# Optimization experiments

Hardware: AMD Instinct MI355X
Metric: run time of the kernel (lower is better)

The kernel has to match this reference:

```python
import jax, jax.numpy as jnp
import numpy as np

# MoE combine: for each sorted row r, output[token_indices[r]] += sorted_gates[r] * expert_outputs[r]
# The EP all_reduce is a sum over the expert-parallel mesh; on a single device it is the identity.

def setup_inputs() -> dict:
    key = jax.random.key(0)
    k1, k2, k3 = jax.random.split(key, 3)
    NUM_TOKENS = 16384   # batch 4 * seq_len 4096
    TOP_K = 2
    D_MODEL = 2048
    NUM_SEL = NUM_TOKENS * TOP_K
    output_buffer = jnp.zeros((NUM_TOKENS, D_MODEL), dtype=jnp.float32)
    expert_outputs = jax.random.normal(k1, (NUM_SEL, D_MODEL), dtype=jnp.float32)
    sorted_gates = jax.random.uniform(k2, (NUM_SEL,), dtype=jnp.float32)
    token_indices = jax.random.randint(k3, (NUM_SEL,), 0, NUM_TOKENS, dtype=jnp.int64)
    return {
        "output_buffer": output_buffer,
        "expert_outputs": expert_outputs,
        "sorted_gates": sorted_gates,
        "token_indices": token_indices,
    }


def reference(output_buffer, expert_outputs, sorted_gates, token_indices):
    # weighted rows: [num_sel, d_model]
    weighted = expert_outputs * sorted_gates[:, None]
    # scatter-add into token slots: [num_tokens, d_model]
    out = output_buffer.at[token_indices].add(weighted)
    # EP all-reduce(sum) is identity on a single device / uninitialized dist.
    return out
```

## Files before the change

### kernel.cpp

```cpp
#include <hip/hip_runtime.h>


static constexpr int NT   = 256;
static constexpr int MAXK = 32;

typedef float fvec4 __attribute__((ext_vector_type(4)));


__global__ void fill_kernel(const int* __restrict__ idx32,
                            const long long* __restrict__ idx64,
                            int* __restrict__ counts,
                            int* __restrict__ slots,
                            int num_sel, int num_tokens) {
    int r = blockIdx.x * blockDim.x + threadIdx.x;
    if (r >= num_sel) return;
    int is64 = 1;
#pragma unroll
    for (int i = 1; i < 32; i += 2) is64 &= (idx32[i] == 0);
    int t = is64 ? (int)idx64[r] : idx32[r];
    if ((unsigned)t >= (unsigned)num_tokens) return;
    int j = atomicAdd(&counts[t], 1);
    if (j < MAXK) slots[t * MAXK + j] = r;
}

__global__ __launch_bounds__(NT) void combine2048_kernel(
    const float* __restrict__ expert,
    const float* __restrict__ gates,
    const int* __restrict__ counts,
    const int* __restrict__ slots,
    float* __restrict__ out) {
    const int b    = blockIdx.x;
    const int t    = b >> 1;
    const int col4 = ((b & 1) * NT + threadIdx.x);
    int c = counts[t];
    if (c > MAXK) c = MAXK;
    const int* sl = slots + t * MAXK;

    fvec4 acc = (fvec4)(0.f);
    for (int j = 0; j < c; ++j) {
        int   r = sl[j];
        float g = gates[r];
        const fvec4* row = (const fvec4*)(expert + (size_t)r * 2048);
        fvec4 e = __builtin_nontemporal_load(row + col4);
        acc.x = fmaf(g, e.x, acc.x);
        acc.y = fmaf(g, e.y, acc.y);
        acc.z = fmaf(g, e.z, acc.z);
        acc.w = fmaf(g, e.w, acc.w);
    }
    fvec4* o = (fvec4*)(out + (size_t)t * 2048);
    __builtin_nontemporal_store(acc, o + col4);
}

__global__ void scatter_atomic_kernel(const float* __restrict__ expert,
                                      const float* __restrict__ gates,
                                      const int* __restrict__ idx32,
                                      const long long* __restrict__ idx64,
                                      float* __restrict__ out,
                                      int d_model, int num_tokens) {
    int r = blockIdx.x;
    int is64 = 1;
#pragma unroll
    for (int i = 1; i < 32; i += 2) is64 &= (idx32[i] == 0);
    int t = is64 ? (int)idx64[r] : idx32[r];
    if ((unsigned)t >= (unsigned)num_tokens) return;
    float g = gates[r];
    const float* row  = expert + (size_t)r * d_model;
    float*       orow = out    + (size_t)t * d_model;
    for (int v = threadIdx.x; v < d_model; v += blockDim.x)
        atomicAdd(&orow[v], g * row[v]);
}

extern "C" void kernel_launch(void* const* d_in, const int* in_sizes, int n_in,
                              void* d_out, int out_size, void* d_ws, size_t ws_size,
                              hipStream_t stream) {
    const float*      expert = (const float*)d_in[1];
    const float*      gates  = (const float*)d_in[2];
    const int*        idx32  = (const int*)d_in[3];
    const long long*  idx64  = (const long long*)d_in[3];
    float*            out    = (float*)d_out;

    const int num_sel    = in_sizes[2];
    const int d_model    = (int)((long long)in_sizes[1] / num_sel);
    const int num_tokens = (int)((long long)out_size / d_model);

    int*  counts = (int*)d_ws;
    int*  slots  = (int*)((char*)d_ws + (size_t)num_tokens * 4);
    const size_t need = (size_t)num_tokens * 4 + (size_t)num_tokens * MAXK * 4;

    if (d_model == 2048 && ws_size >= need) {
        (void)hipMemsetAsync(counts, 0, (size_t)num_tokens * 4, stream);
        fill_kernel<<<(num_sel + NT - 1) / NT, NT, 0, stream>>>(
            idx32, idx64, counts, slots, num_sel, num_tokens);
        combine2048_kernel<<<num_tokens * 2, NT, 0, stream>>>(expert, gates, counts, slots, out);
    } else {
        (void)hipMemsetAsync(d_out, 0, (size_t)out_size * sizeof(float), stream);
        scatter_atomic_kernel<<<num_sel, NT, 0, stream>>>(
            expert, gates, idx32, idx64, out, d_model, num_tokens);
    }
}
```

Before: 435.7 us.

## Borrow output tail as scratch for gather combine and recompute tail rows

The per-token counts and slot lists now live in the last rows of the output buffer instead of the external workspace. This lets the atomic-free gather combine run even when no workspace is supplied, instead of falling back to memset plus a per-element atomicAdd scatter. The combine kernel now handles a full 2048-wide row per block, with two vec4 columns per thread and the row loop unrolled by two. A new rescue kernel recomputes the borrowed tail rows: each of its blocks scans all token indices to find its own rows. That scan is redundant work, but it covers only a few hundred rows.

```diff
diff --git a/kernel.cpp b/kernel.cpp
--- a/kernel.cpp
+++ b/kernel.cpp
@@ -6,6 +6,19 @@
 
 typedef float fvec4 __attribute__((ext_vector_type(4)));
 
+__device__ __forceinline__ void fma4(fvec4& a, float g, fvec4 e) {
+    a.x = fmaf(g, e.x, a.x);
+    a.y = fmaf(g, e.y, a.y);
+    a.z = fmaf(g, e.z, a.z);
+    a.w = fmaf(g, e.w, a.w);
+}
+
+__device__ __forceinline__ int detect_is64(const int* __restrict__ idx32) {
+    int is64 = 1;
+#pragma unroll
+    for (int i = 1; i < 32; i += 2) is64 &= (idx32[i] == 0);
+    return is64;
+}
 
 __global__ void fill_kernel(const int* __restrict__ idx32,
                             const long long* __restrict__ idx64,
@@ -14,9 +27,7 @@
                             int num_sel, int num_tokens) {
     int r = blockIdx.x * blockDim.x + threadIdx.x;
     if (r >= num_sel) return;
-    int is64 = 1;
-#pragma unroll
-    for (int i = 1; i < 32; i += 2) is64 &= (idx32[i] == 0);
+    int is64 = detect_is64(idx32);
     int t = is64 ? (int)idx64[r] : idx32[r];
     if ((unsigned)t >= (unsigned)num_tokens) return;
     int j = atomicAdd(&counts[t], 1);
@@ -29,26 +40,86 @@
     const int* __restrict__ counts,
     const int* __restrict__ slots,
     float* __restrict__ out) {
-    const int b    = blockIdx.x;
-    const int t    = b >> 1;
-    const int col4 = ((b & 1) * NT + threadIdx.x);
+    const int t = blockIdx.x;
     int c = counts[t];
     if (c > MAXK) c = MAXK;
-    const int* sl = slots + t * MAXK;
+    const int* sl = slots + (size_t)t * MAXK;
+    const int q0 = threadIdx.x;
+    const int q1 = threadIdx.x + NT;
 
-    fvec4 acc = (fvec4)(0.f);
-    for (int j = 0; j < c; ++j) {
-        int   r = sl[j];
-        float g = gates[r];
-        const fvec4* row = (const fvec4*)(expert + (size_t)r * 2048);
-        fvec4 e = __builtin_nontemporal_load(row + col4);
-        acc.x = fmaf(g, e.x, acc.x);
-        acc.y = fmaf(g, e.y, acc.y);
-        acc.z = fmaf(g, e.z, acc.z);
-        acc.w = fmaf(g, e.w, acc.w);
+    fvec4 a0 = (fvec4)(0.f), a1 = (fvec4)(0.f);
+    int j = 0;
+    for (; j + 2 <= c; j += 2) {
+        const int   r0 = sl[j];
+        const int   r1 = sl[j + 1];
+        const float g0 = gates[r0];
+        const float g1 = gates[r1];
+        const fvec4* R0 = (const fvec4*)(expert + (size_t)r0 * 2048);
+        const fvec4* R1 = (const fvec4*)(expert + (size_t)r1 * 2048);
+        fvec4 e00 = __builtin_nontemporal_load(R0 + q0);
+        fvec4 e01 = __builtin_nontemporal_load(R0 + q1);
+        fvec4 e10 = __builtin_nontemporal_load(R1 + q0);
+        fvec4 e11 = __builtin_nontemporal_load(R1 + q1);
+        fma4(a0, g0, e00);
+        fma4(a1, g0, e01);
+        fma4(a0, g1, e10);
+        fma4(a1, g1, e11);
+    }
+    if (j < c) {
+        const int   r = sl[j];
+        const float g = gates[r];
+        const fvec4* R = (const fvec4*)(expert + (size_t)r * 2048);
+        fvec4 e0 = __builtin_nontemporal_load(R + q0);
+        fvec4 e1 = __builtin_nontemporal_load(R + q1);
+        fma4(a0, g, e0);
+        fma4(a1, g, e1);
     }
     fvec4* o = (fvec4*)(out + (size_t)t * 2048);
-    __builtin_nontemporal_store(acc, o + col4);
+    __builtin_nontemporal_store(a0, o + q0);
+    __builtin_nontemporal_store(a1, o + q1);
+}
+
+__global__ __launch_bounds__(NT) void rescue2048_kernel(
+    const float* __restrict__ expert,
+    const float* __restrict__ gates,
+    const int* __restrict__ idx32,
+    const long long* __restrict__ idx64,
+    float* __restrict__ out,
+    int num_sel, int t0) {
+    const int t    = t0 + blockIdx.x;
+    const int is64 = detect_is64(idx32);
+
+    __shared__ int   s_r[64];
+    __shared__ float s_g[64];
+    __shared__ int   s_n;
+    if (threadIdx.x == 0) s_n = 0;
+    __syncthreads();
+
+    for (int r = threadIdx.x; r < num_sel; r += NT) {
+        int tt = is64 ? (int)idx64[r] : idx32[r];
+        if (tt == t) {
+            int j = atomicAdd(&s_n, 1);
+            if (j < 64) { s_r[j] = r; s_g[j] = gates[r]; }
+        }
+    }
+    __syncthreads();
+    int n = s_n;
+    if (n > 64) n = 64;
+
+    const int q0 = threadIdx.x, q1 = threadIdx.x + NT;
+    fvec4 a0 = (fvec4)(0.f), a1 = (fvec4)(0.f);
+    for (int j = 0; j < n; ++j) {
+        const int   r = s_r[j];
+        const float g = s_g[j];
+        const fvec4* R = (const fvec4*)(expert + (size_t)r * 2048);
+        fvec4 e0 = __builtin_nontemporal_load(R + q0);
+        fvec4 e1 = __builtin_nontemporal_load(R + q1);
+        fma4(a0, g, e0);
+        fma4(a1, g, e1);
+    }
+    fvec4* o = (fvec4*)(out + (size_t)t * 2048);
+    __builtin_nontemporal_store(a0, o + q0);
+    __builtin_nontemporal_store(a1, o + q1);
 }
 
 __global__ void scatter_atomic_kernel(const float* __restrict__ expert,
@@ -58,9 +129,7 @@
                                       float* __restrict__ out,
                                       int d_model, int num_tokens) {
     int r = blockIdx.x;
-    int is64 = 1;
-#pragma unroll
-    for (int i = 1; i < 32; i += 2) is64 &= (idx32[i] == 0);
+    int is64 = detect_is64(idx32);
     int t = is64 ? (int)idx64[r] : idx32[r];
     if ((unsigned)t >= (unsigned)num_tokens) return;
     float g = gates[r];
@@ -73,6 +142,8 @@
 extern "C" void kernel_launch(void* const* d_in, const int* in_sizes, int n_in,
                               void* d_out, int out_size, void* d_ws, size_t ws_size,
                               hipStream_t stream) {
+    (void)d_ws; (void)ws_size;
+
     const float*      expert = (const float*)d_in[1];
     const float*      gates  = (const float*)d_in[2];
     const int*        idx32  = (const int*)d_in[3];
@@ -83,18 +154,24 @@
     const int d_model    = (int)((long long)in_sizes[1] / num_sel);
     const int num_tokens = (int)((long long)out_size / d_model);
 
-    int*  counts = (int*)d_ws;
-    int*  slots  = (int*)((char*)d_ws + (size_t)num_tokens * 4);
-    const size_t need = (size_t)num_tokens * 4 + (size_t)num_tokens * MAXK * 4;
-
-    if (d_model == 2048 && ws_size >= need) {
-        (void)hipMemsetAsync(counts, 0, (size_t)num_tokens * 4, stream);
-        fill_kernel<<<(num_sel + NT - 1) / NT, NT, 0, stream>>>(
-            idx32, idx64, counts, slots, num_sel, num_tokens);
-        combine2048_kernel<<<num_tokens * 2, NT, 0, stream>>>(expert, gates, counts, slots, out);
-    } else {
-        (void)hipMemsetAsync(d_out, 0, (size_t)out_size * sizeof(float), stream);
-        scatter_atomic_kernel<<<num_sel, NT, 0, stream>>>(
-            expert, gates, idx32, idx64, out, d_model, num_tokens);
+    if (d_model == 2048) {
+        const size_t need  = (size_t)num_tokens * 4u * (1 + MAXK);
+        const size_t rowB  = (size_t)d_model * 4u;
+        const int    R     = (int)((need + rowB - 1) / rowB);
+        const int    t_cut = num_tokens - R;
+        if (t_cut > 0) {
+            int* counts = (int*)(out + (size_t)t_cut * d_model);
+            int* slots  = counts + num_tokens;
+            (void)hipMemsetAsync(counts, 0, (size_t)num_tokens * 4, stream);
+            fill_kernel<<<(num_sel + NT - 1) / NT, NT, 0, stream>>>(
+                idx32, idx64, counts, slots, num_sel, num_tokens);
+            combine2048_kernel<<<t_cut, NT, 0, stream>>>(expert, gates, counts, slots, out);
+            rescue2048_kernel<<<R, NT, 0, stream>>>(expert, gates, idx32, idx64,
+                                                    out, num_sel, t_cut);
+            return;
+        }
     }
+    (void)hipMemsetAsync(d_out, 0, (size_t)out_size * sizeof(float), stream);
+    scatter_atomic_kernel<<<num_sel, NT, 0, stream>>>(
+        expert, gates, idx32, idx64, out, d_model, num_tokens);
 }
```

Result: slower. 478.9 us (+9.9%).
